# Kernel tuning notes

Hardware: AMD Instinct MI355X
Metric: run time of the kernel (lower is better)

## Reference

```python
import jax, jax.numpy as jnp
import numpy as np

B, L, D = 2, 2048, 256
H, DK, DV = 8, 32, 32

def setup_inputs() -> dict:
    key = jax.random.key(0)
    ks = jax.random.split(key, 9)
    s = 1.0 / np.sqrt(D)
    return {
        "q": jax.random.normal(ks[0], (B, L, D), dtype=jnp.float32),
        "k": jax.random.normal(ks[1], (B, L, D), dtype=jnp.float32),
        "v": jax.random.normal(ks[2], (B, L, D), dtype=jnp.float32),
        "w_qs": jax.random.normal(ks[3], (D, H * DK), dtype=jnp.float32) * s,
        "w_ks": jax.random.normal(ks[4], (D, H * DK), dtype=jnp.float32) * s,
        "w_vs": jax.random.normal(ks[5], (D, H * DV), dtype=jnp.float32) * s,
        "w_fc": jax.random.normal(ks[6], (H * DV, D), dtype=jnp.float32) * (1.0 / np.sqrt(H * DV)),
        "ln_gamma": jnp.ones((D,), dtype=jnp.float32),
        "ln_beta": jnp.zeros((D,), dtype=jnp.float32),
    }

def reference(q, k, v, w_qs, w_ks, w_vs, w_fc, ln_gamma, ln_beta):
    residual = q
    temp = jnp.asarray(DK, q.dtype) ** 0.5
    # projections -> [B, H, L, dk/dv]
    qh = (q @ w_qs).reshape(B, L, H, DK).transpose(0, 2, 1, 3)
    kh = (k @ w_ks).reshape(B, L, H, DK).transpose(0, 2, 1, 3)
    vh = (v @ w_vs).reshape(B, L, H, DV).transpose(0, 2, 1, 3)
    # scaled dot-product attention (full score matrix, as in the original)
    scores = jnp.einsum('bhqd,bhkd->bhqk', qh / temp, kh)  # [B,H,L,L]
    attn = jax.nn.softmax(scores, axis=-1)
    out = jnp.einsum('bhqk,bhkd->bhqd', attn, vh)  # [B,H,L,DV]
    out = out.transpose(0, 2, 1, 3).reshape(B, L, H * DV)
    out = out @ w_fc + residual
    # LayerNorm eps=1e-6
    mu = jnp.mean(out, axis=-1, keepdims=True)
    var = jnp.var(out, axis=-1, keepdims=True)
    out = (out - mu) * jax.lax.rsqrt(var + 1e-6) * ln_gamma + ln_beta
    return out, attn
```

## Files before the change

kernel.cpp:

```cpp
#include <hip/hip_runtime.h>
#include <hip/hip_bf16.h>


typedef __bf16 bf16;
typedef __bf16 bf16x8 __attribute__((ext_vector_type(8)));
typedef __bf16 bf16x4 __attribute__((ext_vector_type(4)));
typedef float  f32x4  __attribute__((ext_vector_type(4)));

#define MFMA16(a, b, c) __builtin_amdgcn_mfma_f32_16x16x32_bf16((a), (b), (c), 0, 0, 0)

__device__ __forceinline__ void split_bf16(float x, bf16& hi, bf16& lo) {
    hi = (bf16)x;
    lo = (bf16)(x - (float)hi);
}

__global__ __launch_bounds__(256, 2) void proj_kernel(
    const float* __restrict__ qin, const float* __restrict__ kin, const float* __restrict__ vin,
    const float* __restrict__ wq,  const float* __restrict__ wk,  const float* __restrict__ wv,
    bf16* __restrict__ Qhi, bf16* __restrict__ Qlo,
    bf16* __restrict__ Khi, bf16* __restrict__ Klo, bf16* __restrict__ Vt)
{
    __shared__ bf16 Ah[64][72];
    __shared__ bf16 Al[64][72];
    __shared__ bf16 Bh[64][72];
    __shared__ bf16 Bl[64][72];

    const int proj = blockIdx.y;
    const int tr = blockIdx.x & 63;
    const int tn = blockIdx.x >> 6;
    const float* A = (proj == 0) ? qin : (proj == 1) ? kin : vin;
    const float* W = (proj == 0) ? wq  : (proj == 1) ? wk  : wv;

    const int t = threadIdx.x;
    const int lane = t & 63, w = t >> 6;
    const int m = lane & 15, g = lane >> 4;

    f32x4 acc[2][2] = {};

    for (int kt = 0; kt < 4; ++kt) {
        __syncthreads();
#pragma unroll
        for (int i = 0; i < 4; ++i) {
            int p = t + 256 * i;
            int r = p >> 4;
            int c = (p & 15) << 2;
            float4 f = *(const float4*)&A[(size_t)(tr * 64 + r) * 256 + kt * 64 + c];
            float xs[4] = {f.x, f.y, f.z, f.w};
#pragma unroll
            for (int j = 0; j < 4; ++j) {
                bf16 h, l; split_bf16(xs[j], h, l);
                Ah[r][c + j] = h;
                Al[r][c + j] = l;
            }
        }
#pragma unroll
        for (int i = 0; i < 4; ++i) {
            int p = t + 256 * i;
            int r = p >> 4;
            int c = (p & 15) << 2;
            float4 f = *(const float4*)&W[(size_t)(kt * 64 + r) * 256 + tn * 64 + c];
            float xs[4] = {f.x, f.y, f.z, f.w};
#pragma unroll
            for (int j = 0; j < 4; ++j) {
                bf16 h, l; split_bf16(xs[j], h, l);
                Bh[c + j][r] = h;
                Bl[c + j][r] = l;
            }
        }
        __syncthreads();

#pragma unroll
        for (int ks = 0; ks < 2; ++ks) {
            bf16x8 ah[2], al[2], bh[2], bl[2];
#pragma unroll
            for (int rt = 0; rt < 2; ++rt) {
                int row = ((w >> 1) << 5) + (rt << 4) + m;
                ah[rt] = *(const bf16x8*)&Ah[row][ks * 32 + g * 8];
                al[rt] = *(const bf16x8*)&Al[row][ks * 32 + g * 8];
            }
#pragma unroll
            for (int nt = 0; nt < 2; ++nt) {
                int col = ((w & 1) << 5) + (nt << 4) + m;
                bh[nt] = *(const bf16x8*)&Bh[col][ks * 32 + g * 8];
                bl[nt] = *(const bf16x8*)&Bl[col][ks * 32 + g * 8];
            }
#pragma unroll
            for (int rt = 0; rt < 2; ++rt)
#pragma unroll
                for (int nt = 0; nt < 2; ++nt) {
                    acc[rt][nt] = MFMA16(ah[rt], bh[nt], acc[rt][nt]);
                    acc[rt][nt] = MFMA16(ah[rt], bl[nt], acc[rt][nt]);
                    acc[rt][nt] = MFMA16(al[rt], bh[nt], acc[rt][nt]);
                }
        }
    }

#pragma unroll
    for (int rt = 0; rt < 2; ++rt)
#pragma unroll
        for (int nt = 0; nt < 2; ++nt)
#pragma unroll
            for (int i = 0; i < 4; ++i) {
                int row = tr * 64 + ((w >> 1) << 5) + (rt << 4) + (g << 2) + i;
                int col = tn * 64 + ((w & 1) << 5) + (nt << 4) + m;
                float val = acc[rt][nt][i];
                int b = row >> 11, l2 = row & 2047;
                int hh = col >> 5, d = col & 31;
                int bh8 = b * 8 + hh;
                size_t idx = ((size_t)bh8 * 2048 + l2) * 32 + d;
                if (proj == 0) {
                    bf16 h, l; split_bf16(val * 0.17677669529663688f, h, l);
                    Qhi[idx] = h; Qlo[idx] = l;
                } else if (proj == 1) {
                    bf16 h, l; split_bf16(val, h, l);
                    Khi[idx] = h; Klo[idx] = l;
                } else {
                    Vt[((size_t)bh8 * 32 + d) * 2048 + l2] = (bf16)val;
                }
            }
}

__global__ __launch_bounds__(256) void transpose_wfc(const float* __restrict__ wfc,
                                                     bf16* __restrict__ wt)
{
    __shared__ float tile[32][33];
    const int bk = (blockIdx.x & 7) * 32;
    const int bc = (blockIdx.x >> 3) * 32;
    const int t = threadIdx.x;
    const int c = t & 31, r = t >> 5;
#pragma unroll
    for (int i = 0; i < 4; ++i) {
        int kk = r + i * 8;
        tile[kk][c] = wfc[(size_t)(bk + kk) * 256 + bc + c];
    }
    __syncthreads();
#pragma unroll
    for (int i = 0; i < 4; ++i) {
        int cc = r + i * 8;
        wt[(size_t)(bc + cc) * 256 + bk + c] = (bf16)tile[c][cc];
    }
}

__global__ __launch_bounds__(256, 2) void attn_kernel(
    const bf16* __restrict__ Qhi, const bf16* __restrict__ Qlo,
    const bf16* __restrict__ Khi, const bf16* __restrict__ Klo,
    const bf16* __restrict__ Vt,
    float* __restrict__ attn_out, bf16* __restrict__ out_h)
{
    __shared__ __align__(16) bf16 stage[4][2][16 * 40];

    const int t = threadIdx.x, lane = t & 63, w = t >> 6;
    const int m = lane & 15, g = lane >> 4;
    const int bh = blockIdx.x >> 5;
    const int qb = ((blockIdx.x & 31) << 6) + (w << 4);

    const bf16* Kh = Khi + ((size_t)bh << 16);
    const bf16* Kl = Klo + ((size_t)bh << 16);
    const bf16* Vb = Vt  + ((size_t)bh << 16);

    const size_t qidx = (((size_t)bh << 11) + qb + m) * 32 + g * 8;
    const bf16x8 qh = *(const bf16x8*)&Qhi[qidx];
    const bf16x8 ql = *(const bf16x8*)&Qlo[qidx];

    float rs = 0.f;
    for (int kt = 0; kt < 128; ++kt) {
        const size_t ki = (size_t)(kt * 16 + m) * 32 + g * 8;
        bf16x8 kh = *(const bf16x8*)&Kh[ki];
        bf16x8 kl = *(const bf16x8*)&Kl[ki];
        f32x4 s = {0.f, 0.f, 0.f, 0.f};
        s = MFMA16(kh, qh, s);
        s = MFMA16(kh, ql, s);
        s = MFMA16(kl, qh, s);
        rs += __expf(s[0]) + __expf(s[1]) + __expf(s[2]) + __expf(s[3]);
    }
    rs += __shfl_xor(rs, 16);
    rs += __shfl_xor(rs, 32);
    const float inv = __builtin_amdgcn_rcpf(rs);

    f32x4 o0 = {0.f, 0.f, 0.f, 0.f}, o1 = {0.f, 0.f, 0.f, 0.f};
    float* ab = attn_out + ((size_t)(bh * 2048 + qb + m)) * 2048;

    for (int kt = 0; kt < 64; ++kt) {
        const int key0 = kt << 5;
        const size_t kia = (size_t)(key0 + m) * 32 + g * 8;
        const size_t kib = (size_t)(key0 + 16 + m) * 32 + g * 8;
        bf16x8 kha = *(const bf16x8*)&Kh[kia];
        bf16x8 kla = *(const bf16x8*)&Kl[kia];
        bf16x8 khb = *(const bf16x8*)&Kh[kib];
        bf16x8 klb = *(const bf16x8*)&Kl[kib];

        f32x4 sa = {0.f, 0.f, 0.f, 0.f}, sb = {0.f, 0.f, 0.f, 0.f};
        sa = MFMA16(kha, qh, sa); sa = MFMA16(kha, ql, sa); sa = MFMA16(kla, qh, sa);
        sb = MFMA16(khb, qh, sb); sb = MFMA16(khb, ql, sb); sb = MFMA16(klb, qh, sb);

        f32x4 ea, eb;
#pragma unroll
        for (int i = 0; i < 4; ++i) { ea[i] = __expf(sa[i]); eb[i] = __expf(sb[i]); }

        f32x4 na = {ea[0] * inv, ea[1] * inv, ea[2] * inv, ea[3] * inv};
        f32x4 nb = {eb[0] * inv, eb[1] * inv, eb[2] * inv, eb[3] * inv};
        __builtin_nontemporal_store(na, (f32x4*)&ab[key0 + (g << 2)]);
        __builtin_nontemporal_store(nb, (f32x4*)&ab[key0 + 16 + (g << 2)]);

        bf16x4 pa, pb;
#pragma unroll
        for (int i = 0; i < 4; ++i) { pa[i] = (bf16)ea[i]; pb[i] = (bf16)eb[i]; }
        bf16* sp = &stage[w][kt & 1][0];
        *(bf16x4*)&sp[m * 40 + (g << 2)] = pa;
        *(bf16x4*)&sp[m * 40 + 16 + (g << 2)] = pb;
        bf16x8 pf = *(const bf16x8*)&sp[m * 40 + (g << 3)];

        bf16x8 v0 = *(const bf16x8*)&Vb[(size_t)m * 2048 + key0 + (g << 3)];
        bf16x8 v1 = *(const bf16x8*)&Vb[(size_t)(m + 16) * 2048 + key0 + (g << 3)];
        o0 = MFMA16(pf, v0, o0);
        o1 = MFMA16(pf, v1, o1);
    }

    const int b = bh >> 3, hh = bh & 7;
#pragma unroll
    for (int i = 0; i < 4; ++i) {
        float invq = __shfl(inv, (g << 2) + i);
        size_t base = ((size_t)b * 2048 + qb + (g << 2) + i) * 256 + hh * 32;
        out_h[base + m]      = (bf16)(o0[i] * invq);
        out_h[base + 16 + m] = (bf16)(o1[i] * invq);
    }
}

__global__ __launch_bounds__(256, 2) void fc_ln_kernel(
    const bf16* __restrict__ oh, const bf16* __restrict__ wt,
    const float* __restrict__ qres, const float* __restrict__ gamma,
    const float* __restrict__ beta, float* __restrict__ outp)
{
    __shared__ float tile[16][260];
    const int rbase = blockIdx.x << 4;
    const int t = threadIdx.x, lane = t & 63, w = t >> 6;
    const int m = lane & 15, g = lane >> 4;

    f32x4 acc[4] = {};
#pragma unroll
    for (int ks = 0; ks < 8; ++ks) {
        bf16x8 a = *(const bf16x8*)&oh[(size_t)(rbase + m) * 256 + ks * 32 + g * 8];
#pragma unroll
        for (int ct = 0; ct < 4; ++ct) {
            int col = (w << 6) + (ct << 4) + m;
            bf16x8 bb = *(const bf16x8*)&wt[(size_t)col * 256 + ks * 32 + g * 8];
            acc[ct] = MFMA16(a, bb, acc[ct]);
        }
    }
#pragma unroll
    for (int ct = 0; ct < 4; ++ct)
#pragma unroll
        for (int i = 0; i < 4; ++i) {
            int row = (g << 2) + i;
            int col = (w << 6) + (ct << 4) + m;
            tile[row][col] = acc[ct][i] + qres[(size_t)(rbase + row) * 256 + col];
        }
    __syncthreads();

#pragma unroll
    for (int rr = 0; rr < 4; ++rr) {
        int row = (w << 2) + rr;
        int c = lane << 2;
        float4 x = *(const float4*)&tile[row][c];
        float s  = x.x + x.y + x.z + x.w;
        float sq = x.x * x.x + x.y * x.y + x.z * x.z + x.w * x.w;
#pragma unroll
        for (int off = 1; off < 64; off <<= 1) {
            s  += __shfl_xor(s, off);
            sq += __shfl_xor(sq, off);
        }
        float mu   = s * (1.0f / 256.0f);
        float var  = sq * (1.0f / 256.0f) - mu * mu;
        float rstd = rsqrtf(var + 1e-6f);
        float4 gm = *(const float4*)&gamma[c];
        float4 bt = *(const float4*)&beta[c];
        float4 y;
        y.x = (x.x - mu) * rstd * gm.x + bt.x;
        y.y = (x.y - mu) * rstd * gm.y + bt.y;
        y.z = (x.z - mu) * rstd * gm.z + bt.z;
        y.w = (x.w - mu) * rstd * gm.w + bt.w;
        *(float4*)&outp[(size_t)(rbase + row) * 256 + c] = y;
    }
}

extern "C" void kernel_launch(void* const* d_in, const int* in_sizes, int n_in,
                              void* d_out, int out_size, void* d_ws, size_t ws_size,
                              hipStream_t stream)
{
    (void)in_sizes; (void)n_in; (void)out_size; (void)ws_size;

    const float* q   = (const float*)d_in[0];
    const float* k   = (const float*)d_in[1];
    const float* v   = (const float*)d_in[2];
    const float* wq  = (const float*)d_in[3];
    const float* wk  = (const float*)d_in[4];
    const float* wv  = (const float*)d_in[5];
    const float* wfc = (const float*)d_in[6];
    const float* gm  = (const float*)d_in[7];
    const float* bt  = (const float*)d_in[8];

    float* out  = (float*)d_out;
    float* attn = out + (size_t)2 * 2048 * 256;

    char* ws = (char*)d_ws;
    bf16* Qhi = (bf16*)(ws);
    bf16* Qlo = (bf16*)(ws + ((size_t)2 << 20));
    bf16* Khi = (bf16*)(ws + ((size_t)4 << 20));
    bf16* Klo = (bf16*)(ws + ((size_t)6 << 20));
    bf16* Vt  = (bf16*)(ws + ((size_t)8 << 20));
    bf16* oh  = (bf16*)(ws + ((size_t)10 << 20));
    bf16* wt  = (bf16*)(ws + ((size_t)12 << 20));

    proj_kernel<<<dim3(256, 3), 256, 0, stream>>>(q, k, v, wq, wk, wv,
                                                  Qhi, Qlo, Khi, Klo, Vt);
    transpose_wfc<<<64, 256, 0, stream>>>(wfc, wt);
    attn_kernel<<<512, 256, 0, stream>>>(Qhi, Qlo, Khi, Klo, Vt, attn, oh);
    fc_ln_kernel<<<256, 256, 0, stream>>>(oh, wt, q, gm, bt, out);
}
```

Baseline: 386.6 us.

## Pre-split and transpose projection weights once, load MFMA operands directly from global

A new prep kernel transposes the Q/K/V weights and splits them into bf16 hi/lo pairs, and it also takes over the existing w_fc transpose. The projection kernel then drops its shared-memory staging and barriers, loading A rows and pre-split weight rows straight from global into MFMA registers, with an occupancy hint raised to 3. This removes repeated per-block fp32-to-bf16 splitting of weights and LDS traffic and synchronisation. In exchange, each wave re-reads global memory without sharing tiles across the block, so it relies on cache hits. The projection stage is likely a small share of total time next to the attention kernel.

```diff
diff --git a/kernel.cpp b/kernel.cpp
--- a/kernel.cpp
+++ b/kernel.cpp
@@ -14,85 +14,97 @@
     lo = (bf16)(x - (float)hi);
 }
 
-__global__ __launch_bounds__(256, 2) void proj_kernel(
+__global__ __launch_bounds__(256) void prep_weights(
+    const float* __restrict__ wq, const float* __restrict__ wk,
+    const float* __restrict__ wv, const float* __restrict__ wfc,
+    bf16* __restrict__ Wqh, bf16* __restrict__ Wql,
+    bf16* __restrict__ Wkh, bf16* __restrict__ Wkl,
+    bf16* __restrict__ Wvh, bf16* __restrict__ Wvl,
+    bf16* __restrict__ wt)
+{
+    __shared__ float tile[32][33];
+    const int mat = blockIdx.y;
+    const float* src = (mat == 0) ? wq : (mat == 1) ? wk : (mat == 2) ? wv : wfc;
+    const int bk = (blockIdx.x & 7) * 32;
+    const int bc = (blockIdx.x >> 3) * 32;
+    const int t = threadIdx.x;
+    const int c = t & 31, r = t >> 5;
+#pragma unroll
+    for (int i = 0; i < 4; ++i) {
+        int kk = r + i * 8;
+        tile[kk][c] = src[(size_t)(bk + kk) * 256 + bc + c];
+    }
+    __syncthreads();
+#pragma unroll
+    for (int i = 0; i < 4; ++i) {
+        int nn = r + i * 8;
+        float x = tile[c][nn];
+        size_t idx = (size_t)(bc + nn) * 256 + bk + c;
+        if (mat == 3) {
+            wt[idx] = (bf16)x;
+        } else {
+            bf16 h, l; split_bf16(x, h, l);
+            bf16* H = (mat == 0) ? Wqh : (mat == 1) ? Wkh : Wvh;
+            bf16* L = (mat == 0) ? Wql : (mat == 1) ? Wkl : Wvl;
+            H[idx] = h; L[idx] = l;
+        }
+    }
+}
+
+__global__ __launch_bounds__(256, 3) void proj_kernel(
     const float* __restrict__ qin, const float* __restrict__ kin, const float* __restrict__ vin,
-    const float* __restrict__ wq,  const float* __restrict__ wk,  const float* __restrict__ wv,
+    const bf16* __restrict__ Wqh, const bf16* __restrict__ Wql,
+    const bf16* __restrict__ Wkh, const bf16* __restrict__ Wkl,
+    const bf16* __restrict__ Wvh, const bf16* __restrict__ Wvl,
     bf16* __restrict__ Qhi, bf16* __restrict__ Qlo,
     bf16* __restrict__ Khi, bf16* __restrict__ Klo, bf16* __restrict__ Vt)
 {
-    __shared__ bf16 Ah[64][72];
-    __shared__ bf16 Al[64][72];
-    __shared__ bf16 Bh[64][72];
-    __shared__ bf16 Bl[64][72];
-
     const int proj = blockIdx.y;
     const int tr = blockIdx.x & 63;
     const int tn = blockIdx.x >> 6;
-    const float* A = (proj == 0) ? qin : (proj == 1) ? kin : vin;
-    const float* W = (proj == 0) ? wq  : (proj == 1) ? wk  : wv;
+    const float* A  = (proj == 0) ? qin : (proj == 1) ? kin : vin;
+    const bf16*  WH = (proj == 0) ? Wqh : (proj == 1) ? Wkh : Wvh;
+    const bf16*  WL = (proj == 0) ? Wql : (proj == 1) ? Wkl : Wvl;
 
     const int t = threadIdx.x;
     const int lane = t & 63, w = t >> 6;
     const int m = lane & 15, g = lane >> 4;
 
+    const int row0 = tr * 64 + ((w >> 1) << 5);
+    const int col0 = tn * 64 + ((w & 1) << 5);
+
     f32x4 acc[2][2] = {};
 
-    for (int kt = 0; kt < 4; ++kt) {
-        __syncthreads();
-#pragma unroll
-        for (int i = 0; i < 4; ++i) {
-            int p = t + 256 * i;
-            int r = p >> 4;
-            int c = (p & 15) << 2;
-            float4 f = *(const float4*)&A[(size_t)(tr * 64 + r) * 256 + kt * 64 + c];
-            float xs[4] = {f.x, f.y, f.z, f.w};
-#pragma unroll
-            for (int j = 0; j < 4; ++j) {
+#pragma unroll
+    for (int ks = 0; ks < 8; ++ks) {
+        const int k0 = ks * 32 + g * 8;
+        bf16x8 ah[2], al[2], bh[2], bl[2];
+#pragma unroll
+        for (int rt = 0; rt < 2; ++rt) {
+            const float* ap = &A[(size_t)(row0 + (rt << 4) + m) * 256 + k0];
+            float4 f0 = *(const float4*)ap;
+            float4 f1 = *(const float4*)(ap + 4);
+            float xs[8] = {f0.x, f0.y, f0.z, f0.w, f1.x, f1.y, f1.z, f1.w};
+#pragma unroll
+            for (int j = 0; j < 8; ++j) {
                 bf16 h, l; split_bf16(xs[j], h, l);
-                Ah[r][c + j] = h;
-                Al[r][c + j] = l;
+                ah[rt][j] = h; al[rt][j] = l;
             }
         }
 #pragma unroll
-        for (int i = 0; i < 4; ++i) {
-            int p = t + 256 * i;
-            int r = p >> 4;
-            int c = (p & 15) << 2;
-            float4 f = *(const float4*)&W[(size_t)(kt * 64 + r) * 256 + tn * 64 + c];
-            float xs[4] = {f.x, f.y, f.z, f.w};
-#pragma unroll
-            for (int j = 0; j < 4; ++j) {
-                bf16 h, l; split_bf16(xs[j], h, l);
-                Bh[c + j][r] = h;
-                Bl[c + j][r] = l;
+        for (int nt = 0; nt < 2; ++nt) {
+            size_t wi = (size_t)(col0 + (nt << 4) + m) * 256 + k0;
+            bh[nt] = *(const bf16x8*)&WH[wi];
+            bl[nt] = *(const bf16x8*)&WL[wi];
+        }
+#pragma unroll
+        for (int rt = 0; rt < 2; ++rt)
+#pragma unroll
+            for (int nt = 0; nt < 2; ++nt) {
+                acc[rt][nt] = MFMA16(ah[rt], bh[nt], acc[rt][nt]);
+                acc[rt][nt] = MFMA16(ah[rt], bl[nt], acc[rt][nt]);
+                acc[rt][nt] = MFMA16(al[rt], bh[nt], acc[rt][nt]);
             }
-        }
-        __syncthreads();
-
-#pragma unroll
-        for (int ks = 0; ks < 2; ++ks) {
-            bf16x8 ah[2], al[2], bh[2], bl[2];
-#pragma unroll
-            for (int rt = 0; rt < 2; ++rt) {
-                int row = ((w >> 1) << 5) + (rt << 4) + m;
-                ah[rt] = *(const bf16x8*)&Ah[row][ks * 32 + g * 8];
-                al[rt] = *(const bf16x8*)&Al[row][ks * 32 + g * 8];
-            }
-#pragma unroll
-            for (int nt = 0; nt < 2; ++nt) {
-                int col = ((w & 1) << 5) + (nt << 4) + m;
-                bh[nt] = *(const bf16x8*)&Bh[col][ks * 32 + g * 8];
-                bl[nt] = *(const bf16x8*)&Bl[col][ks * 32 + g * 8];
-            }
-#pragma unroll
-            for (int rt = 0; rt < 2; ++rt)
-#pragma unroll
-                for (int nt = 0; nt < 2; ++nt) {
-                    acc[rt][nt] = MFMA16(ah[rt], bh[nt], acc[rt][nt]);
-                    acc[rt][nt] = MFMA16(ah[rt], bl[nt], acc[rt][nt]);
-                    acc[rt][nt] = MFMA16(al[rt], bh[nt], acc[rt][nt]);
-                }
-        }
     }
 
 #pragma unroll
@@ -120,27 +132,6 @@
             }
 }
 
-__global__ __launch_bounds__(256) void transpose_wfc(const float* __restrict__ wfc,
-                                                     bf16* __restrict__ wt)
-{
-    __shared__ float tile[32][33];
-    const int bk = (blockIdx.x & 7) * 32;
-    const int bc = (blockIdx.x >> 3) * 32;
-    const int t = threadIdx.x;
-    const int c = t & 31, r = t >> 5;
-#pragma unroll
-    for (int i = 0; i < 4; ++i) {
-        int kk = r + i * 8;
-        tile[kk][c] = wfc[(size_t)(bk + kk) * 256 + bc + c];
-    }
-    __syncthreads();
-#pragma unroll
-    for (int i = 0; i < 4; ++i) {
-        int cc = r + i * 8;
-        wt[(size_t)(bc + cc) * 256 + bk + c] = (bf16)tile[c][cc];
-    }
-}
-
 __global__ __launch_bounds__(256, 2) void attn_kernel(
     const bf16* __restrict__ Qhi, const bf16* __restrict__ Qlo,
     const bf16* __restrict__ Khi, const bf16* __restrict__ Klo,
@@ -310,10 +301,18 @@
     bf16* Vt  = (bf16*)(ws + ((size_t)8 << 20));
     bf16* oh  = (bf16*)(ws + ((size_t)10 << 20));
     bf16* wt  = (bf16*)(ws + ((size_t)12 << 20));
-
-    proj_kernel<<<dim3(256, 3), 256, 0, stream>>>(q, k, v, wq, wk, wv,
+    bf16* Wqh = (bf16*)(ws + ((size_t)12 << 20) + (1 << 17));
+    bf16* Wql = (bf16*)(ws + ((size_t)12 << 20) + (2 << 17));
+    bf16* Wkh = (bf16*)(ws + ((size_t)12 << 20) + (3 << 17));
+    bf16* Wkl = (bf16*)(ws + ((size_t)12 << 20) + (4 << 17));
+    bf16* Wvh = (bf16*)(ws + ((size_t)12 << 20) + (5 << 17));
+    bf16* Wvl = (bf16*)(ws + ((size_t)12 << 20) + (6 << 17));
+
+    prep_weights<<<dim3(64, 4), 256, 0, stream>>>(wq, wk, wv, wfc,
+                                                  Wqh, Wql, Wkh, Wkl, Wvh, Wvl, wt);
+    proj_kernel<<<dim3(256, 3), 256, 0, stream>>>(q, k, v,
+                                                  Wqh, Wql, Wkh, Wkl, Wvh, Wvl,
                                                   Qhi, Qlo, Khi, Klo, Vt);
-    transpose_wfc<<<64, 256, 0, stream>>>(wfc, wt);
     attn_kernel<<<512, 256, 0, stream>>>(Qhi, Qlo, Khi, Klo, Vt, attn, oh);
     fc_ln_kernel<<<256, 256, 0, stream>>>(oh, wt, q, gm, bt, out);
 }
```

Result: no change. 385.2 us (-0.4%).
